# Optimization experiments

Measured on AMD Instinct MI355X. Metric: run time of the kernel, lower is better.

Reference implementation:

```python
import jax, jax.numpy as jnp
import numpy as np

N, E, D, T = 100000, 1600000, 128, 5
EPS = 1e-5


def setup_inputs() -> dict:
    key = jax.random.key(0)
    ks = jax.random.split(key, 8)
    scale = 1.0 / np.sqrt(D)
    return {
        "features": jax.random.normal(ks[0], (N, D), dtype=jnp.float32),
        "src": jax.random.randint(ks[1], (E,), 0, N, dtype=jnp.int32),
        "dst": jax.random.randint(ks[2], (E,), 0, N, dtype=jnp.int32),
        "etype": jax.random.randint(ks[3], (E,), 0, T, dtype=jnp.int32),
        "w1": jax.random.normal(ks[4], (T * D, D), dtype=jnp.float32) * scale,
        "b1": jnp.zeros((T * D,), dtype=jnp.float32),
        "g1": jnp.ones((D,), dtype=jnp.float32),
        "be1": jnp.zeros((D,), dtype=jnp.float32),
        "w2": jax.random.normal(ks[5], (T * D, D), dtype=jnp.float32) * scale,
        "b2": jnp.zeros((T * D,), dtype=jnp.float32),
        "g2": jnp.ones((D,), dtype=jnp.float32),
        "be2": jnp.zeros((D,), dtype=jnp.float32),
    }


def _bn(x, gamma, beta):
    # BatchNorm1d in training mode: biased batch statistics over node axis.
    mu = jnp.mean(x, axis=0)
    var = jnp.mean((x - mu) ** 2, axis=0)
    return gamma * (x - mu) * jax.lax.rsqrt(var + EPS) + beta


def _round(x, w, b, gamma, beta, src, dst, etype):
    h = jax.nn.relu(_bn(x, gamma, beta))
    h = jnp.einsum('nd,od->no', h, w) + b          # [N, T*D]
    h3 = h.reshape(N, T, D)
    # one-hot multiply + sum over types == select the etype slice per edge
    msg = h3[src, etype]                            # [E, D] gather
    return jax.ops.segment_sum(msg, dst, num_segments=N)  # [N, D] scatter-add


def reference(features, src, dst, etype, w1, b1, g1, be1, w2, b2, g2, be2):
    h_new = _round(features, w1, b1, g1, be1, src, dst, etype)
    h_new = _round(h_new, w2, b2, g2, be2, src, dst, etype)
    return h_new + features
```

## Files before the change

kernel.cpp:

```cpp
#include <hip/hip_runtime.h>

#define NN 100000
#define EE 1600000
#define DD 128
#define TD 640
#define EPSV 1e-5f
#define NBLK_SCAN 391
#define SB 1024
#define NRANGE 8
#define RSZ 12500
#define NCHUNK 256
#define CSZ 6250

typedef __attribute__((ext_vector_type(8))) short bf16x8;
typedef __attribute__((ext_vector_type(4))) float f32x4;
typedef const __attribute__((address_space(1))) unsigned int gu32;
typedef __attribute__((address_space(3))) unsigned int lu32;

__device__ inline unsigned short f2b(float f) {
  union { float f; unsigned u; } x; x.f = f;
  unsigned r = x.u + 0x7fff + ((x.u >> 16) & 1);
  return (unsigned short)(r >> 16);
}
__device__ inline float b2f(unsigned short u) {
  union { unsigned u; float f; } x; x.u = ((unsigned)u) << 16;
  return x.f;
}

__global__ __launch_bounds__(256) void k_stats_partial(const float* __restrict__ x,
    float* __restrict__ ps, float* __restrict__ pq) {
  float s0=0.f,s1=0.f,s2=0.f,s3=0.f,q0=0.f,q1=0.f,q2=0.f,q3=0.f;
  const float4* x4 = reinterpret_cast<const float4*>(x);
  const int total = NN * DD / 4;
  for (int i = blockIdx.x * 256 + threadIdx.x; i < total; i += SB * 256) {
    float4 v = x4[i];
    s0 += v.x; s1 += v.y; s2 += v.z; s3 += v.w;
    q0 += v.x*v.x; q1 += v.y*v.y; q2 += v.z*v.z; q3 += v.w*v.w;
  }
  __shared__ float ls[256], lq[256];
  int t = threadIdx.x;
  float sv[4] = {s0,s1,s2,s3}, qv[4] = {q0,q1,q2,q3};
#pragma unroll
  for (int j = 0; j < 4; ++j) {
    ls[t] = sv[j]; lq[t] = qv[j];
    __syncthreads();
    if (t < 32) {
      float a = 0.f, b = 0.f;
#pragma unroll
      for (int k = 0; k < 8; ++k) { a += ls[t + 32*k]; b += lq[t + 32*k]; }
      ps[blockIdx.x * DD + t*4 + j] = a;
      pq[blockIdx.x * DD + t*4 + j] = b;
    }
    __syncthreads();
  }
}

__global__ __launch_bounds__(256) void k_stats_partial_bf(const unsigned short* __restrict__ x,
    float* __restrict__ ps, float* __restrict__ pq) {
  float s0=0.f,s1=0.f,s2=0.f,s3=0.f,q0=0.f,q1=0.f,q2=0.f,q3=0.f;
  const ushort4* x4 = reinterpret_cast<const ushort4*>(x);
  const int total = NN * DD / 4;
  for (int i = blockIdx.x * 256 + threadIdx.x; i < total; i += SB * 256) {
    ushort4 u = x4[i];
    float vx = b2f(u.x), vy = b2f(u.y), vz = b2f(u.z), vw = b2f(u.w);
    s0 += vx; s1 += vy; s2 += vz; s3 += vw;
    q0 += vx*vx; q1 += vy*vy; q2 += vz*vz; q3 += vw*vw;
  }
  __shared__ float ls[256], lq[256];
  int t = threadIdx.x;
  float sv[4] = {s0,s1,s2,s3}, qv[4] = {q0,q1,q2,q3};
#pragma unroll
  for (int j = 0; j < 4; ++j) {
    ls[t] = sv[j]; lq[t] = qv[j];
    __syncthreads();
    if (t < 32) {
      float a = 0.f, b = 0.f;
#pragma unroll
      for (int k = 0; k < 8; ++k) { a += ls[t + 32*k]; b += lq[t + 32*k]; }
      ps[blockIdx.x * DD + t*4 + j] = a;
      pq[blockIdx.x * DD + t*4 + j] = b;
    }
    __syncthreads();
  }
}

__global__ __launch_bounds__(1024) void k_stats_final(const float* __restrict__ ps,
    const float* __restrict__ pq, const float* __restrict__ g,
    const float* __restrict__ be, float* __restrict__ ssb) {
  __shared__ float ls[1024], lq[1024];
  int t = threadIdx.x;
  int col = t & 127, seg = t >> 7;
  float s = 0.f, q = 0.f;
  for (int b = seg; b < SB; b += 8) { s += ps[b * DD + col]; q += pq[b * DD + col]; }
  ls[t] = s; lq[t] = q;
  __syncthreads();
  if (t < 128) {
#pragma unroll
    for (int k = 1; k < 8; ++k) { s += ls[t + 128*k]; q += lq[t + 128*k]; }
    float mean = s * (1.0f / NN);
    float var  = q * (1.0f / NN) - mean * mean;
    float sc = g[t] * rsqrtf(var + EPSV);
    ssb[t] = sc;
    ssb[DD + t] = be[t] - mean * sc;
  }
}

__global__ __launch_bounds__(256) void k_act(const float* __restrict__ x,
    const float* __restrict__ ss, unsigned short* __restrict__ A) {
  int i = blockIdx.x * 256 + threadIdx.x;
  float4 v = reinterpret_cast<const float4*>(x)[i];
  int c4 = (i & 31) * 4;
  float s0 = ss[c4+0], s1 = ss[c4+1], s2 = ss[c4+2], s3 = ss[c4+3];
  float h0 = ss[DD+c4+0], h1 = ss[DD+c4+1], h2 = ss[DD+c4+2], h3 = ss[DD+c4+3];
  ushort4 o;
  o.x = f2b(fmaxf(0.f, v.x * s0 + h0));
  o.y = f2b(fmaxf(0.f, v.y * s1 + h1));
  o.z = f2b(fmaxf(0.f, v.z * s2 + h2));
  o.w = f2b(fmaxf(0.f, v.w * s3 + h3));
  reinterpret_cast<ushort4*>(A)[i] = o;
}

__global__ __launch_bounds__(256) void k_act_bf(const unsigned short* __restrict__ x,
    const float* __restrict__ ss, unsigned short* __restrict__ A) {
  int i = blockIdx.x * 256 + threadIdx.x;
  ushort4 u = reinterpret_cast<const ushort4*>(x)[i];
  int c4 = (i & 31) * 4;
  float s0 = ss[c4+0], s1 = ss[c4+1], s2 = ss[c4+2], s3 = ss[c4+3];
  float h0 = ss[DD+c4+0], h1 = ss[DD+c4+1], h2 = ss[DD+c4+2], h3 = ss[DD+c4+3];
  ushort4 o;
  o.x = f2b(fmaxf(0.f, b2f(u.x) * s0 + h0));
  o.y = f2b(fmaxf(0.f, b2f(u.y) * s1 + h1));
  o.z = f2b(fmaxf(0.f, b2f(u.z) * s2 + h2));
  o.w = f2b(fmaxf(0.f, b2f(u.w) * s3 + h3));
  reinterpret_cast<ushort4*>(A)[i] = o;
}

__global__ void k_cvt_b2(const float* __restrict__ w1, unsigned short* __restrict__ o1,
                         const float* __restrict__ w2, unsigned short* __restrict__ o2) {
  int bi = blockIdx.x;
  const float* w = (bi < 80) ? w1 : w2;
  unsigned short* o = (bi < 80) ? o1 : o2;
  if (bi >= 80) bi -= 80;
  int i = bi * 256 + threadIdx.x;
  int tt = i >> 12;
  int rem = i & 4095;
  int d = rem >> 5, j = rem & 31;
  float4 v = reinterpret_cast<const float4*>(w)[i];
  ushort4 u; u.x = f2b(v.x); u.y = f2b(v.y); u.z = f2b(v.z); u.w = f2b(v.w);
  int u16 = tt * 16 + (j >> 1);
  int u16s = (u16 & ~7) | ((u16 & 7) ^ (d & 7));
  reinterpret_cast<ushort4*>(o)[d * 160 + u16s * 2 + (j & 1)] = u;
}

__global__ void k_zero(int* p, int n) {
  int i = blockIdx.x * 256 + threadIdx.x;
  if (i < n) p[i] = 0;
}
__global__ __launch_bounds__(256) void k_hist(const int* __restrict__ dst,
    int* __restrict__ cnt) {
  const int range = blockIdx.x & (NRANGE - 1);
  const int chunk = blockIdx.x >> 3;
  const int lo = range * RSZ;
  const int base = chunk * CSZ;
  for (int i = base + threadIdx.x; i < base + CSZ; i += 256) {
    int d = dst[i];
    if ((unsigned)(d - lo) < RSZ) atomicAdd(&cnt[d], 1);
  }
}
__global__ __launch_bounds__(256) void k_scan_blk(const int* __restrict__ cnt, int* __restrict__ bsum) {
  __shared__ int sh[256];
  int idx = blockIdx.x * 256 + threadIdx.x;
  sh[threadIdx.x] = (idx < NN) ? cnt[idx] : 0;
  __syncthreads();
  for (int off = 128; off > 0; off >>= 1) {
    if (threadIdx.x < off) sh[threadIdx.x] += sh[threadIdx.x + off];
    __syncthreads();
  }
  if (threadIdx.x == 0) bsum[blockIdx.x] = sh[0];
}
__global__ __launch_bounds__(512) void k_scan_top(int* __restrict__ bsum) {
  __shared__ int sh[512];
  int t = threadIdx.x;
  int v = (t < NBLK_SCAN) ? bsum[t] : 0;
  sh[t] = v;
  __syncthreads();
  for (int off = 1; off < 512; off <<= 1) {
    int add = (t >= off) ? sh[t - off] : 0;
    __syncthreads();
    sh[t] += add;
    __syncthreads();
  }
  if (t < NBLK_SCAN) bsum[t] = sh[t] - v;
}
__global__ __launch_bounds__(256) void k_scan_fin(const int* __restrict__ cnt,
    const int* __restrict__ bsum, int* __restrict__ row_ptr, int* __restrict__ cursor) {
  __shared__ int sh[256];
  int idx = blockIdx.x * 256 + threadIdx.x;
  int v = (idx < NN) ? cnt[idx] : 0;
  sh[threadIdx.x] = v;
  __syncthreads();
  for (int off = 1; off < 256; off <<= 1) {
    int add = (threadIdx.x >= off) ? sh[threadIdx.x - off] : 0;
    __syncthreads();
    sh[threadIdx.x] += add;
    __syncthreads();
  }
  int excl = bsum[blockIdx.x] + sh[threadIdx.x] - v;
  if (idx < NN) { row_ptr[idx] = excl; cursor[idx] = excl; }
  if (idx == NN - 1) row_ptr[NN] = excl + v;
}
__global__ __launch_bounds__(256) void k_scatter(const int* __restrict__ src,
    const int* __restrict__ dst, const int* __restrict__ et,
    int* __restrict__ cursor, int* __restrict__ payload) {
  const int range = blockIdx.x & (NRANGE - 1);
  const int chunk = blockIdx.x >> 3;
  const int lo = range * RSZ;
  const int base = chunk * CSZ;
  for (int i = base + threadIdx.x; i < base + CSZ; i += 256) {
    int d = dst[i];
    if ((unsigned)(d - lo) < RSZ) {
      int pos = atomicAdd(&cursor[d], 1);
      payload[pos] = (src[i] << 3) | et[i];
    }
  }
}

__global__ __launch_bounds__(256) void k_agg(const unsigned short* __restrict__ Ab,
    const int* __restrict__ rp, const int* __restrict__ pl,
    unsigned short* __restrict__ G, int* __restrict__ cntb) {
  const int n = blockIdx.x * 4 + (threadIdx.x >> 6);
  const int l = threadIdx.x & 63;
  const int s = __builtin_amdgcn_readfirstlane(rp[n]);
  const int e = __builtin_amdgcn_readfirstlane(rp[n + 1]);
  float a00=0.f,a01=0.f,a10=0.f,a11=0.f,a20=0.f,a21=0.f,a30=0.f,a31=0.f,a40=0.f,a41=0.f;
  int c0=0,c1=0,c2=0,c3=0,c4=0;
  int j = s;
#define ACC_ONE(P, U) do {                                              \
    float x0 = b2f((U).x), x1 = b2f((U).y);                             \
    switch ((P) & 7) {                                                  \
      case 0: a00 += x0; a01 += x1; c0++; break;                        \
      case 1: a10 += x0; a11 += x1; c1++; break;                        \
      case 2: a20 += x0; a21 += x1; c2++; break;                        \
      case 3: a30 += x0; a31 += x1; c3++; break;                        \
      default: a40 += x0; a41 += x1; c4++; break;                       \
    } } while (0)
  int p0=0,p1=0,p2=0,p3=0,p4=0,p5=0,p6=0,p7=0;
  if (j + 7 < e) {
    p0 = __builtin_amdgcn_readfirstlane(pl[j]);
    p1 = __builtin_amdgcn_readfirstlane(pl[j + 1]);
    p2 = __builtin_amdgcn_readfirstlane(pl[j + 2]);
    p3 = __builtin_amdgcn_readfirstlane(pl[j + 3]);
    p4 = __builtin_amdgcn_readfirstlane(pl[j + 4]);
    p5 = __builtin_amdgcn_readfirstlane(pl[j + 5]);
    p6 = __builtin_amdgcn_readfirstlane(pl[j + 6]);
    p7 = __builtin_amdgcn_readfirstlane(pl[j + 7]);
  }
  for (; j + 15 < e; j += 8) {
    ushort2 u0 = *reinterpret_cast<const ushort2*>(Ab + (p0 >> 3) * DD + 2 * l);
    ushort2 u1 = *reinterpret_cast<const ushort2*>(Ab + (p1 >> 3) * DD + 2 * l);
    ushort2 u2 = *reinterpret_cast<const ushort2*>(Ab + (p2 >> 3) * DD + 2 * l);
    ushort2 u3 = *reinterpret_cast<const ushort2*>(Ab + (p3 >> 3) * DD + 2 * l);
    ushort2 u4 = *reinterpret_cast<const ushort2*>(Ab + (p4 >> 3) * DD + 2 * l);
    ushort2 u5 = *reinterpret_cast<const ushort2*>(Ab + (p5 >> 3) * DD + 2 * l);
    ushort2 u6 = *reinterpret_cast<const ushort2*>(Ab + (p6 >> 3) * DD + 2 * l);
    ushort2 u7 = *reinterpret_cast<const ushort2*>(Ab + (p7 >> 3) * DD + 2 * l);
    int q0 = __builtin_amdgcn_readfirstlane(pl[j + 8]);
    int q1 = __builtin_amdgcn_readfirstlane(pl[j + 9]);
    int q2 = __builtin_amdgcn_readfirstlane(pl[j + 10]);
    int q3 = __builtin_amdgcn_readfirstlane(pl[j + 11]);
    int q4 = __builtin_amdgcn_readfirstlane(pl[j + 12]);
    int q5 = __builtin_amdgcn_readfirstlane(pl[j + 13]);
    int q6 = __builtin_amdgcn_readfirstlane(pl[j + 14]);
    int q7 = __builtin_amdgcn_readfirstlane(pl[j + 15]);
    ACC_ONE(p0, u0); ACC_ONE(p1, u1); ACC_ONE(p2, u2); ACC_ONE(p3, u3);
    ACC_ONE(p4, u4); ACC_ONE(p5, u5); ACC_ONE(p6, u6); ACC_ONE(p7, u7);
    p0=q0; p1=q1; p2=q2; p3=q3; p4=q4; p5=q5; p6=q6; p7=q7;
  }
  if (j + 7 < e) {
    ushort2 u0 = *reinterpret_cast<const ushort2*>(Ab + (p0 >> 3) * DD + 2 * l);
    ushort2 u1 = *reinterpret_cast<const ushort2*>(Ab + (p1 >> 3) * DD + 2 * l);
    ushort2 u2 = *reinterpret_cast<const ushort2*>(Ab + (p2 >> 3) * DD + 2 * l);
    ushort2 u3 = *reinterpret_cast<const ushort2*>(Ab + (p3 >> 3) * DD + 2 * l);
    ushort2 u4 = *reinterpret_cast<const ushort2*>(Ab + (p4 >> 3) * DD + 2 * l);
    ushort2 u5 = *reinterpret_cast<const ushort2*>(Ab + (p5 >> 3) * DD + 2 * l);
    ushort2 u6 = *reinterpret_cast<const ushort2*>(Ab + (p6 >> 3) * DD + 2 * l);
    ushort2 u7 = *reinterpret_cast<const ushort2*>(Ab + (p7 >> 3) * DD + 2 * l);
    ACC_ONE(p0, u0); ACC_ONE(p1, u1); ACC_ONE(p2, u2); ACC_ONE(p3, u3);
    ACC_ONE(p4, u4); ACC_ONE(p5, u5); ACC_ONE(p6, u6); ACC_ONE(p7, u7);
    j += 8;
  }
  for (; j < e; ++j) {
    int p = __builtin_amdgcn_readfirstlane(pl[j]);
    ushort2 u = *reinterpret_cast<const ushort2*>(Ab + (p >> 3) * DD + 2 * l);
    ACC_ONE(p, u);
  }
#undef ACC_ONE
  unsigned short* gp = G + n * TD + 2 * l;
  ushort2 o;
  o.x = f2b(a00); o.y = f2b(a01); *reinterpret_cast<ushort2*>(gp + 0 * DD) = o;
  o.x = f2b(a10); o.y = f2b(a11); *reinterpret_cast<ushort2*>(gp + 1 * DD) = o;
  o.x = f2b(a20); o.y = f2b(a21); *reinterpret_cast<ushort2*>(gp + 2 * DD) = o;
  o.x = f2b(a30); o.y = f2b(a31); *reinterpret_cast<ushort2*>(gp + 3 * DD) = o;
  o.x = f2b(a40); o.y = f2b(a41); *reinterpret_cast<ushort2*>(gp + 4 * DD) = o;
  if (l < 5) {
    int c = (l == 0) ? c0 : (l == 1) ? c1 : (l == 2) ? c2 : (l == 3) ? c3 : c4;
    cntb[n * 8 + l] = c;
  }
}

template<int RND>
__global__ __launch_bounds__(256, 4) void k_gemm2(const unsigned short* __restrict__ G,
    const unsigned short* __restrict__ B2, const float* __restrict__ bias,
    const int* __restrict__ cntb, const float* __restrict__ base,
    void* __restrict__ out) {
  __shared__ __align__(16) unsigned short wlds[2][8192];
  const int t = threadIdx.x;
  const int l = t & 63;
  const int w = t >> 6;
  const int lm = l & 15, hi = l >> 4;
  const int R = blockIdx.x * 128;
  const char* b2c = reinterpret_cast<const char*>(B2);

#define STAGE(BUF, KS) do {                                                    \
    _Pragma("unroll") for (int k = 0; k < 4; ++k) {                            \
      int idx = k * 256 + t;                                                   \
      int c = idx >> 3, sub = idx & 7;                                         \
      __builtin_amdgcn_global_load_lds(                                        \
          (gu32*)(b2c + c * 1280 + (KS) * 128 + sub * 16),                     \
          (lu32*)(reinterpret_cast<char*>(wlds[BUF]) + (k * 256 + (t & ~63)) * 16), \
          16, 0, 0);                                                           \
    }                                                                          \
  } while (0)

  STAGE(0, 0);
  __syncthreads();

  const unsigned short* ap[2];
#pragma unroll
  for (int rf = 0; rf < 2; ++rf) {
    int ar = R + w * 32 + rf * 16 + lm; if (ar >= NN) ar = NN - 1;
    ap[rf] = G + ar * TD + hi * 8;
  }

  f32x4 acc[2][8] = {};
#pragma unroll 1
  for (int ks = 0; ks < 10; ++ks) {
    const int buf = ks & 1;
    if (ks < 9) STAGE(buf ^ 1, ks + 1);
    bf16x8 af[2][2];
#pragma unroll
    for (int rf = 0; rf < 2; ++rf) {
      af[rf][0] = *reinterpret_cast<const bf16x8*>(ap[rf] + ks * 64);
      af[rf][1] = *reinterpret_cast<const bf16x8*>(ap[rf] + ks * 64 + 32);
    }
    char* bc = (char*)wlds[buf];
    const unsigned sw = (unsigned)((lm & 7) << 4);
#pragma unroll
    for (int cf = 0; cf < 8; ++cf) {
      int colB = cf * 16 + lm;
      bf16x8 b0 = *reinterpret_cast<const bf16x8*>(bc + colB * 128 + ((hi * 16) ^ sw));
      bf16x8 b1 = *reinterpret_cast<const bf16x8*>(bc + colB * 128 + ((64 + hi * 16) ^ sw));
#pragma unroll
      for (int rf = 0; rf < 2; ++rf) {
        acc[rf][cf] = __builtin_amdgcn_mfma_f32_16x16x32_bf16(af[rf][0], b0, acc[rf][cf], 0, 0, 0);
        acc[rf][cf] = __builtin_amdgcn_mfma_f32_16x16x32_bf16(af[rf][1], b1, acc[rf][cf], 0, 0, 0);
      }
    }
    __syncthreads();
  }
#undef STAGE

#pragma unroll
  for (int cf = 0; cf < 8; ++cf) {
    int col = cf * 16 + lm;
    float bb0 = bias[col], bb1 = bias[128 + col], bb2 = bias[256 + col],
          bb3 = bias[384 + col], bb4 = bias[512 + col];
#pragma unroll
    for (int rf = 0; rf < 2; ++rf) {
#pragma unroll
      for (int r = 0; r < 4; ++r) {
        int row = R + w * 32 + rf * 16 + hi * 4 + r;
        if (row < NN) {
          const int* cp = cntb + row * 8;
          float v = acc[rf][cf][r] + cp[0]*bb0 + cp[1]*bb1 + cp[2]*bb2 + cp[3]*bb3 + cp[4]*bb4;
          if (RND == 1) {
            v += base[row * DD + col];
            reinterpret_cast<float*>(out)[row * DD + col] = v;
          } else {
            reinterpret_cast<unsigned short*>(out)[row * DD + col] = f2b(v);
          }
        }
      }
    }
  }
}

extern "C" void kernel_launch(void* const* d_in, const int* in_sizes, int n_in,
                              void* d_out, int out_size, void* d_ws, size_t ws_size,
                              hipStream_t stream) {
  const float* features = (const float*)d_in[0];
  const int*   src   = (const int*)d_in[1];
  const int*   dst   = (const int*)d_in[2];
  const int*   etype = (const int*)d_in[3];
  const float* w1  = (const float*)d_in[4];
  const float* b1  = (const float*)d_in[5];
  const float* g1  = (const float*)d_in[6];
  const float* be1 = (const float*)d_in[7];
  const float* w2  = (const float*)d_in[8];
  const float* b2  = (const float*)d_in[9];
  const float* g2  = (const float*)d_in[10];
  const float* be2 = (const float*)d_in[11];

  char* ws = (char*)d_ws;
  unsigned short* Ab   = (unsigned short*)(ws + 0);
  float*          ps   = (float*)(ws + 0);
  float*          pq   = (float*)(ws + 524288);
  unsigned short* G    = (unsigned short*)(ws + 25600000);
  unsigned short* y1   = (unsigned short*)(ws + 153600000);
  unsigned short* b2a  = (unsigned short*)(ws + 179200000);
  unsigned short* b2b  = (unsigned short*)(ws + 179363840);
  float*          ssb  = (float*)(ws + 179527680);
  int*            rowp = (int*)(ws + 179528704);
  int*            curs = (int*)(ws + 179928720);
  int*            payl = (int*)(ws + 180328720);
  int*            bsum = (int*)(ws + 186728720);
  int*            cntb = (int*)(ws + 186730768);

  k_zero<<<(NN + 255) / 256, 256, 0, stream>>>(curs, NN);
  k_hist<<<NRANGE * NCHUNK, 256, 0, stream>>>(dst, curs);
  k_scan_blk<<<NBLK_SCAN, 256, 0, stream>>>(curs, bsum);
  k_scan_top<<<1, 512, 0, stream>>>(bsum);
  k_scan_fin<<<NBLK_SCAN, 256, 0, stream>>>(curs, bsum, rowp, curs);
  k_scatter<<<NRANGE * NCHUNK, 256, 0, stream>>>(src, dst, etype, curs, payl);

  k_cvt_b2<<<160, 256, 0, stream>>>(w1, b2a, w2, b2b);

  k_stats_partial<<<SB, 256, 0, stream>>>(features, ps, pq);
  k_stats_final<<<1, 1024, 0, stream>>>(ps, pq, g1, be1, ssb);
  k_act<<<12500, 256, 0, stream>>>(features, ssb, Ab);
  k_agg<<<NN / 4, 256, 0, stream>>>(Ab, rowp, payl, G, cntb);
  k_gemm2<0><<<782, 256, 0, stream>>>(G, b2a, b1, cntb, nullptr, y1);

  k_stats_partial_bf<<<SB, 256, 0, stream>>>(y1, ps, pq);
  k_stats_final<<<1, 1024, 0, stream>>>(ps, pq, g2, be2, ssb);
  k_act_bf<<<12500, 256, 0, stream>>>(y1, ssb, Ab);
  k_agg<<<NN / 4, 256, 0, stream>>>(Ab, rowp, payl, G, cntb);
  k_gemm2<1><<<782, 256, 0, stream>>>(G, b2b, b2, cntb, features, d_out);
}
```

Before: 543.4 us.

## Merge independent setup kernels and fuse round-two BN statistics into the GEMM epilogue

Independent preprocessing kernels (cursor zeroing, feature statistics, weight conversion) are packed into one launch that dispatches on block index. The histogram is merged with the first BN finalisation, and the scan finish is merged with the first activation. The round-one GEMM epilogue now accumulates per-column sums and sums of squares into per-block partials, which removes the separate pass that re-read y1 for round-two statistics. The fused statistics use fp32 values before bf16 rounding, so results can differ slightly from the old path, and the epilogue gains extra LDS work and a barrier.

```diff
diff --git a/kernel.cpp b/kernel.cpp
--- a/kernel.cpp
+++ b/kernel.cpp
@@ -11,6 +11,7 @@
 #define RSZ 12500
 #define NCHUNK 256
 #define CSZ 6250
+#define GB2 782
 
 typedef __attribute__((ext_vector_type(8))) short bf16x8;
 typedef __attribute__((ext_vector_type(4))) float f32x4;
@@ -27,76 +28,83 @@
   return x.f;
 }
 
-__global__ __launch_bounds__(256) void k_stats_partial(const float* __restrict__ x,
-    float* __restrict__ ps, float* __restrict__ pq) {
-  float s0=0.f,s1=0.f,s2=0.f,s3=0.f,q0=0.f,q1=0.f,q2=0.f,q3=0.f;
-  const float4* x4 = reinterpret_cast<const float4*>(x);
-  const int total = NN * DD / 4;
-  for (int i = blockIdx.x * 256 + threadIdx.x; i < total; i += SB * 256) {
-    float4 v = x4[i];
-    s0 += v.x; s1 += v.y; s2 += v.z; s3 += v.w;
-    q0 += v.x*v.x; q1 += v.y*v.y; q2 += v.z*v.z; q3 += v.w*v.w;
+__global__ __launch_bounds__(256) void k_pre1(int* __restrict__ curs,
+    const float* __restrict__ x, float* __restrict__ ps, float* __restrict__ pq,
+    const float* __restrict__ w1, unsigned short* __restrict__ o1,
+    const float* __restrict__ w2, unsigned short* __restrict__ o2) {
+  const int bi = blockIdx.x;
+  const int t = threadIdx.x;
+  if (bi < NBLK_SCAN) {
+    int i = bi * 256 + t;
+    if (i < NN) curs[i] = 0;
+    return;
+  }
+  if (bi < NBLK_SCAN + SB) {
+    const int sb = bi - NBLK_SCAN;
+    float s0=0.f,s1=0.f,s2=0.f,s3=0.f,q0=0.f,q1=0.f,q2=0.f,q3=0.f;
+    const float4* x4 = reinterpret_cast<const float4*>(x);
+    const int total = NN * DD / 4;
+    for (int i = sb * 256 + t; i < total; i += SB * 256) {
+      float4 v = x4[i];
+      s0 += v.x; s1 += v.y; s2 += v.z; s3 += v.w;
+      q0 += v.x*v.x; q1 += v.y*v.y; q2 += v.z*v.z; q3 += v.w*v.w;
+    }
+    __shared__ float ls[256], lq[256];
+    float sv[4] = {s0,s1,s2,s3}, qv[4] = {q0,q1,q2,q3};
+#pragma unroll
+    for (int j = 0; j < 4; ++j) {
+      ls[t] = sv[j]; lq[t] = qv[j];
+      __syncthreads();
+      if (t < 32) {
+        float a = 0.f, b = 0.f;
+#pragma unroll
+        for (int k = 0; k < 8; ++k) { a += ls[t + 32*k]; b += lq[t + 32*k]; }
+        ps[sb * DD + t*4 + j] = a;
+        pq[sb * DD + t*4 + j] = b;
+      }
+      __syncthreads();
+    }
+    return;
+  }
+  int cb = bi - (NBLK_SCAN + SB);
+  const float* w = (cb < 80) ? w1 : w2;
+  unsigned short* o = (cb < 80) ? o1 : o2;
+  if (cb >= 80) cb -= 80;
+  int i = cb * 256 + t;
+  int tt = i >> 12;
+  int rem = i & 4095;
+  int d = rem >> 5, j = rem & 31;
+  float4 v = reinterpret_cast<const float4*>(w)[i];
+  ushort4 u; u.x = f2b(v.x); u.y = f2b(v.y); u.z = f2b(v.z); u.w = f2b(v.w);
+  int u16 = tt * 16 + (j >> 1);
+  int u16s = (u16 & ~7) | ((u16 & 7) ^ (d & 7));
+  reinterpret_cast<ushort4*>(o)[d * 160 + u16s * 2 + (j & 1)] = u;
+}
+
+__global__ __launch_bounds__(256) void k_pre2(const int* __restrict__ dst,
+    int* __restrict__ cnt, const float* __restrict__ ps, const float* __restrict__ pq,
+    const float* __restrict__ g, const float* __restrict__ be, float* __restrict__ ssb) {
+  const int bi = blockIdx.x;
+  const int t = threadIdx.x;
+  if (bi < NRANGE * NCHUNK) {
+    const int range = bi & (NRANGE - 1);
+    const int chunk = bi >> 3;
+    const int lo = range * RSZ;
+    const int base = chunk * CSZ;
+    for (int i = base + t; i < base + CSZ; i += 256) {
+      int d = dst[i];
+      if ((unsigned)(d - lo) < RSZ) atomicAdd(&cnt[d], 1);
+    }
+    return;
   }
   __shared__ float ls[256], lq[256];
-  int t = threadIdx.x;
-  float sv[4] = {s0,s1,s2,s3}, qv[4] = {q0,q1,q2,q3};
-#pragma unroll
-  for (int j = 0; j < 4; ++j) {
-    ls[t] = sv[j]; lq[t] = qv[j];
-    __syncthreads();
-    if (t < 32) {
-      float a = 0.f, b = 0.f;
-#pragma unroll
-      for (int k = 0; k < 8; ++k) { a += ls[t + 32*k]; b += lq[t + 32*k]; }
-      ps[blockIdx.x * DD + t*4 + j] = a;
-      pq[blockIdx.x * DD + t*4 + j] = b;
-    }
-    __syncthreads();
-  }
-}
-
-__global__ __launch_bounds__(256) void k_stats_partial_bf(const unsigned short* __restrict__ x,
-    float* __restrict__ ps, float* __restrict__ pq) {
-  float s0=0.f,s1=0.f,s2=0.f,s3=0.f,q0=0.f,q1=0.f,q2=0.f,q3=0.f;
-  const ushort4* x4 = reinterpret_cast<const ushort4*>(x);
-  const int total = NN * DD / 4;
-  for (int i = blockIdx.x * 256 + threadIdx.x; i < total; i += SB * 256) {
-    ushort4 u = x4[i];
-    float vx = b2f(u.x), vy = b2f(u.y), vz = b2f(u.z), vw = b2f(u.w);
-    s0 += vx; s1 += vy; s2 += vz; s3 += vw;
-    q0 += vx*vx; q1 += vy*vy; q2 += vz*vz; q3 += vw*vw;
-  }
-  __shared__ float ls[256], lq[256];
-  int t = threadIdx.x;
-  float sv[4] = {s0,s1,s2,s3}, qv[4] = {q0,q1,q2,q3};
-#pragma unroll
-  for (int j = 0; j < 4; ++j) {
-    ls[t] = sv[j]; lq[t] = qv[j];
-    __syncthreads();
-    if (t < 32) {
-      float a = 0.f, b = 0.f;
-#pragma unroll
-      for (int k = 0; k < 8; ++k) { a += ls[t + 32*k]; b += lq[t + 32*k]; }
-      ps[blockIdx.x * DD + t*4 + j] = a;
-      pq[blockIdx.x * DD + t*4 + j] = b;
-    }
-    __syncthreads();
-  }
-}
-
-__global__ __launch_bounds__(1024) void k_stats_final(const float* __restrict__ ps,
-    const float* __restrict__ pq, const float* __restrict__ g,
-    const float* __restrict__ be, float* __restrict__ ssb) {
-  __shared__ float ls[1024], lq[1024];
-  int t = threadIdx.x;
   int col = t & 127, seg = t >> 7;
   float s = 0.f, q = 0.f;
-  for (int b = seg; b < SB; b += 8) { s += ps[b * DD + col]; q += pq[b * DD + col]; }
+  for (int b = seg; b < SB; b += 2) { s += ps[b * DD + col]; q += pq[b * DD + col]; }
   ls[t] = s; lq[t] = q;
   __syncthreads();
   if (t < 128) {
-#pragma unroll
-    for (int k = 1; k < 8; ++k) { s += ls[t + 128*k]; q += lq[t + 128*k]; }
+    s = ls[t] + ls[t + 128]; q = lq[t] + lq[t + 128];
     float mean = s * (1.0f / NN);
     float var  = q * (1.0f / NN) - mean * mean;
     float sc = g[t] * rsqrtf(var + EPSV);
@@ -105,9 +113,50 @@
   }
 }
 
-__global__ __launch_bounds__(256) void k_act(const float* __restrict__ x,
-    const float* __restrict__ ss, unsigned short* __restrict__ A) {
-  int i = blockIdx.x * 256 + threadIdx.x;
+__global__ __launch_bounds__(256) void k_stats_final2(const float* __restrict__ ps,
+    const float* __restrict__ pq, const float* __restrict__ g,
+    const float* __restrict__ be, float* __restrict__ ssb) {
+  __shared__ float ls[256], lq[256];
+  int t = threadIdx.x;
+  int col = t & 127, seg = t >> 7;
+  float s = 0.f, q = 0.f;
+  for (int b = seg; b < GB2; b += 2) { s += ps[b * DD + col]; q += pq[b * DD + col]; }
+  ls[t] = s; lq[t] = q;
+  __syncthreads();
+  if (t < 128) {
+    s = ls[t] + ls[t + 128]; q = lq[t] + lq[t + 128];
+    float mean = s * (1.0f / NN);
+    float var  = q * (1.0f / NN) - mean * mean;
+    float sc = g[t] * rsqrtf(var + EPSV);
+    ssb[t] = sc;
+    ssb[DD + t] = be[t] - mean * sc;
+  }
+}
+
+__global__ __launch_bounds__(256) void k_mid(const int* __restrict__ cnt,
+    const int* __restrict__ bsum, int* __restrict__ row_ptr, int* __restrict__ cursor,
+    const float* __restrict__ x, const float* __restrict__ ss,
+    unsigned short* __restrict__ A) {
+  const int bi = blockIdx.x;
+  const int t = threadIdx.x;
+  if (bi < NBLK_SCAN) {
+    __shared__ int sh[256];
+    int idx = bi * 256 + t;
+    int v = (idx < NN) ? cnt[idx] : 0;
+    sh[t] = v;
+    __syncthreads();
+    for (int off = 1; off < 256; off <<= 1) {
+      int add = (t >= off) ? sh[t - off] : 0;
+      __syncthreads();
+      sh[t] += add;
+      __syncthreads();
+    }
+    int excl = bsum[bi] + sh[t] - v;
+    if (idx < NN) { row_ptr[idx] = excl; cursor[idx] = excl; }
+    if (idx == NN - 1) row_ptr[NN] = excl + v;
+    return;
+  }
+  int i = (bi - NBLK_SCAN) * 256 + t;
   float4 v = reinterpret_cast<const float4*>(x)[i];
   int c4 = (i & 31) * 4;
   float s0 = ss[c4+0], s1 = ss[c4+1], s2 = ss[c4+2], s3 = ss[c4+3];
@@ -135,38 +184,6 @@
   reinterpret_cast<ushort4*>(A)[i] = o;
 }
 
-__global__ void k_cvt_b2(const float* __restrict__ w1, unsigned short* __restrict__ o1,
-                         const float* __restrict__ w2, unsigned short* __restrict__ o2) {
-  int bi = blockIdx.x;
-  const float* w = (bi < 80) ? w1 : w2;
-  unsigned short* o = (bi < 80) ? o1 : o2;
-  if (bi >= 80) bi -= 80;
-  int i = bi * 256 + threadIdx.x;
-  int tt = i >> 12;
-  int rem = i & 4095;
-  int d = rem >> 5, j = rem & 31;
-  float4 v = reinterpret_cast<const float4*>(w)[i];
-  ushort4 u; u.x = f2b(v.x); u.y = f2b(v.y); u.z = f2b(v.z); u.w = f2b(v.w);
-  int u16 = tt * 16 + (j >> 1);
-  int u16s = (u16 & ~7) | ((u16 & 7) ^ (d & 7));
-  reinterpret_cast<ushort4*>(o)[d * 160 + u16s * 2 + (j & 1)] = u;
-}
-
-__global__ void k_zero(int* p, int n) {
-  int i = blockIdx.x * 256 + threadIdx.x;
-  if (i < n) p[i] = 0;
-}
-__global__ __launch_bounds__(256) void k_hist(const int* __restrict__ dst,
-    int* __restrict__ cnt) {
-  const int range = blockIdx.x & (NRANGE - 1);
-  const int chunk = blockIdx.x >> 3;
-  const int lo = range * RSZ;
-  const int base = chunk * CSZ;
-  for (int i = base + threadIdx.x; i < base + CSZ; i += 256) {
-    int d = dst[i];
-    if ((unsigned)(d - lo) < RSZ) atomicAdd(&cnt[d], 1);
-  }
-}
 __global__ __launch_bounds__(256) void k_scan_blk(const int* __restrict__ cnt, int* __restrict__ bsum) {
   __shared__ int sh[256];
   int idx = blockIdx.x * 256 + threadIdx.x;
@@ -191,23 +208,6 @@
     __syncthreads();
   }
   if (t < NBLK_SCAN) bsum[t] = sh[t] - v;
-}
-__global__ __launch_bounds__(256) void k_scan_fin(const int* __restrict__ cnt,
-    const int* __restrict__ bsum, int* __restrict__ row_ptr, int* __restrict__ cursor) {
-  __shared__ int sh[256];
-  int idx = blockIdx.x * 256 + threadIdx.x;
-  int v = (idx < NN) ? cnt[idx] : 0;
-  sh[threadIdx.x] = v;
-  __syncthreads();
-  for (int off = 1; off < 256; off <<= 1) {
-    int add = (threadIdx.x >= off) ? sh[threadIdx.x - off] : 0;
-    __syncthreads();
-    sh[threadIdx.x] += add;
-    __syncthreads();
-  }
-  int excl = bsum[blockIdx.x] + sh[threadIdx.x] - v;
-  if (idx < NN) { row_ptr[idx] = excl; cursor[idx] = excl; }
-  if (idx == NN - 1) row_ptr[NN] = excl + v;
 }
 __global__ __launch_bounds__(256) void k_scatter(const int* __restrict__ src,
     const int* __restrict__ dst, const int* __restrict__ et,
@@ -312,7 +312,7 @@
 __global__ __launch_bounds__(256, 4) void k_gemm2(const unsigned short* __restrict__ G,
     const unsigned short* __restrict__ B2, const float* __restrict__ bias,
     const int* __restrict__ cntb, const float* __restrict__ base,
-    void* __restrict__ out) {
+    void* __restrict__ out, float* __restrict__ ps2, float* __restrict__ pq2) {
   __shared__ __align__(16) unsigned short wlds[2][8192];
   const int t = threadIdx.x;
   const int l = t & 63;
@@ -370,6 +370,7 @@
   }
 #undef STAGE
 
+  float sv[8] = {}, qv[8] = {};
 #pragma unroll
   for (int cf = 0; cf < 8; ++cf) {
     int col = cf * 16 + lm;
@@ -388,9 +389,29 @@
             reinterpret_cast<float*>(out)[row * DD + col] = v;
           } else {
             reinterpret_cast<unsigned short*>(out)[row * DD + col] = f2b(v);
+            sv[cf] += v; qv[cf] += v * v;
           }
         }
       }
+    }
+  }
+  if (RND == 0) {
+    float* rs = reinterpret_cast<float*>(wlds[0]);
+    float* rq = reinterpret_cast<float*>(wlds[1]);
+    const int slot = w * 4 + hi;
+#pragma unroll
+    for (int cf = 0; cf < 8; ++cf) {
+      int col = cf * 16 + lm;
+      rs[col * 16 + slot] = sv[cf];
+      rq[col * 16 + slot] = qv[cf];
+    }
+    __syncthreads();
+    if (t < 128) {
+      float s = 0.f, q = 0.f;
+#pragma unroll
+      for (int k = 0; k < 16; ++k) { s += rs[t * 16 + k]; q += rq[t * 16 + k]; }
+      ps2[blockIdx.x * DD + t] = s;
+      pq2[blockIdx.x * DD + t] = q;
     }
   }
 }
@@ -426,24 +447,20 @@
   int*            bsum = (int*)(ws + 186728720);
   int*            cntb = (int*)(ws + 186730768);
 
-  k_zero<<<(NN + 255) / 256, 256, 0, stream>>>(curs, NN);
-  k_hist<<<NRANGE * NCHUNK, 256, 0, stream>>>(dst, curs);
+  k_pre1<<<NBLK_SCAN + SB + 160, 256, 0, stream>>>(curs, features, ps, pq,
+                                                   w1, b2a, w2, b2b);
+  k_pre2<<<NRANGE * NCHUNK + 1, 256, 0, stream>>>(dst, curs, ps, pq, g1, be1, ssb);
   k_scan_blk<<<NBLK_SCAN, 256, 0, stream>>>(curs, bsum);
   k_scan_top<<<1, 512, 0, stream>>>(bsum);
-  k_scan_fin<<<NBLK_SCAN, 256, 0, stream>>>(curs, bsum, rowp, curs);
+  k_mid<<<NBLK_SCAN + 12500, 256, 0, stream>>>(curs, bsum, rowp, curs,
+                                               features, ssb, Ab);
   k_scatter<<<NRANGE * NCHUNK, 256, 0, stream>>>(src, dst, etype, curs, payl);
 
-  k_cvt_b2<<<160, 256, 0, stream>>>(w1, b2a, w2, b2b);
-
-  k_stats_partial<<<SB, 256, 0, stream>>>(features, ps, pq);
-  k_stats_final<<<1, 1024, 0, stream>>>(ps, pq, g1, be1, ssb);
-  k_act<<<12500, 256, 0, stream>>>(features, ssb, Ab);
   k_agg<<<NN / 4, 256, 0, stream>>>(Ab, rowp, payl, G, cntb);
-  k_gemm2<0><<<782, 256, 0, stream>>>(G, b2a, b1, cntb, nullptr, y1);
-
-  k_stats_partial_bf<<<SB, 256, 0, stream>>>(y1, ps, pq);
-  k_stats_final<<<1, 1024, 0, stream>>>(ps, pq, g2, be2, ssb);
+  k_gemm2<0><<<GB2, 256, 0, stream>>>(G, b2a, b1, cntb, nullptr, y1, ps, pq);
+
+  k_stats_final2<<<1, 256, 0, stream>>>(ps, pq, g2, be2, ssb);
   k_act_bf<<<12500, 256, 0, stream>>>(y1, ssb, Ab);
   k_agg<<<NN / 4, 256, 0, stream>>>(Ab, rowp, payl, G, cntb);
-  k_gemm2<1><<<782, 256, 0, stream>>>(G, b2b, b2, cntb, features, d_out);
-}
+  k_gemm2<1><<<GB2, 256, 0, stream>>>(G, b2b, b2, cntb, features, d_out, nullptr, nullptr);
+}
```

Result: slower. 679.5 us (+25.1%).
